# Kernel optimization log

Hardware: AMD Instinct MI355X
Metric: run time of the kernel (lower is better)

Reference implementation:

```python
import jax, jax.numpy as jnp
import numpy as np

B, S, D = 4, 2048, 1024
H = 16
HD = D // H  # 64


def setup_inputs() -> dict:
    key = jax.random.key(0)
    ks = jax.random.split(key, 5)
    std = 1.0 / np.sqrt(D)
    return {
        "x": jax.random.normal(ks[0], (B, S, D), dtype=jnp.float32),
        "Wq": jax.random.normal(ks[1], (D, D), dtype=jnp.float32) * std,
        "Wk": jax.random.normal(ks[2], (D, D), dtype=jnp.float32) * std,
        "Wv": jax.random.normal(ks[3], (D, D), dtype=jnp.float32) * std,
        "Wo": jax.random.normal(ks[4], (D, D), dtype=jnp.float32) * std,
        "bo": jnp.zeros((D,), dtype=jnp.float32),
    }


def reference(x, Wq, Wk, Wv, Wo, bo):
    b, n, d_in = x.shape
    q = (x @ Wq).reshape(b, n, H, HD).transpose(0, 2, 1, 3)  # [b,h,n,hd]
    k = (x @ Wk).reshape(b, n, H, HD).transpose(0, 2, 1, 3)
    v = (x @ Wv).reshape(b, n, H, HD).transpose(0, 2, 1, 3)
    scores = jnp.einsum("bhqd,bhkd->bhqk", q, k)  # full NxN, as in original
    causal = jnp.tril(jnp.ones((n, n), dtype=bool))  # True = keep
    scores = jnp.where(causal, scores, -jnp.inf)
    attn = jax.nn.softmax(scores / np.sqrt(HD), axis=-1)
    # dropout p=0.0 -> identity
    ctx = jnp.einsum("bhqk,bhkd->bqhd", attn, v).reshape(b, n, H * HD)
    return ctx @ Wo + bo
```

## Files before the change

### kernel.cpp

```cpp
#include <hip/hip_runtime.h>
#include <math.h>

#define BATCH 4
#define SLEN 2048
#define DMODEL 1024
#define NH 16
#define HD 64
#define MROWS (BATCH * SLEN)
#define QK_LD 2048

typedef __attribute__((ext_vector_type(8))) short short8;
typedef __attribute__((ext_vector_type(4))) float floatx4;

#define AS1 __attribute__((address_space(1)))
#define AS3 __attribute__((address_space(3)))

__device__ inline unsigned short f2bf(float f) {
    union { float f; unsigned u; } a; a.f = f;
    unsigned r = a.u + 0x7fff + ((a.u >> 16) & 1);
    return (unsigned short)(r >> 16);
}

__device__ inline unsigned pack_bf(float lo, float hi) {
    union { float f; unsigned u; } a, b; a.f = lo; b.f = hi;
    return __builtin_amdgcn_perm(b.u + 0x8000u, a.u + 0x8000u, 0x07060302u);
}
__device__ inline unsigned pack_tr(float lo, float hi) {
    union { float f; unsigned u; } a, b; a.f = lo; b.f = hi;
    return __builtin_amdgcn_perm(b.u, a.u, 0x07060302u);
}

__global__ __launch_bounds__(256) void cvt_all(
    const float* __restrict__ x,
    const float* __restrict__ Wq, const float* __restrict__ Wk,
    const float* __restrict__ Wv, const float* __restrict__ Wo,
    short* __restrict__ xb,
    short* __restrict__ WqkT, short* __restrict__ WvT, short* __restrict__ WoT)
{
    int bid = blockIdx.x;
    if (bid < 8192) {
        int i = (bid * 256 + threadIdx.x) * 4;
        float4 v = *(const float4*)(x + i);
        unsigned short t0 = f2bf(v.x), t1 = f2bf(v.y), t2 = f2bf(v.z), t3 = f2bf(v.w);
        uint2 o;
        o.x = (unsigned)t0 | ((unsigned)t1 << 16);
        o.y = (unsigned)t2 | ((unsigned)t3 << 16);
        *(uint2*)(xb + i) = o;
    } else {
        bid -= 8192;
        int z = bid >> 10;
        int inner = bid & 1023;
        int bxi = inner & 31, byi = inner >> 5;

        const float* W; short* Wt; float sc = 1.0f;
        if (z == 0)      { W = Wq; Wt = WqkT; sc = 0.18033688011112042f; }
        else if (z == 1) { W = Wk; Wt = WqkT + (size_t)DMODEL * DMODEL; }
        else if (z == 2) { W = Wv; Wt = WvT; }
        else             { W = Wo; Wt = WoT; }

        __shared__ float t[32][33];
        int bn = bxi * 32, bk = byi * 32;
        int tx = threadIdx.x & 31, r0 = (threadIdx.x >> 5) * 4;
        #pragma unroll
        for (int i = 0; i < 4; i++)
            t[r0 + i][tx] = W[(size_t)(bk + r0 + i) * DMODEL + bn + tx];
        __syncthreads();
        #pragma unroll
        for (int i = 0; i < 4; i++)
            Wt[(size_t)(bn + r0 + i) * DMODEL + bk + tx] = (short)f2bf(t[tx][r0 + i] * sc);
    }
}

#define TM 128
#define TN 128
#define TK 32

template <int OUT_BF16>
__device__ __forceinline__ void gemm_body(
    const short* __restrict__ A,
    const short* __restrict__ Bt,
    const float* __restrict__ bias,
    void* __restrict__ Cout, int N, int K, int m0, int n0)
{
    __shared__ short As[2][TM * TK];
    __shared__ short Bs[2][TN * TK];
    int tid = threadIdx.x;
    int l = tid & 63, w = tid >> 6;
    int wm = (w >> 1) * 64, wn = (w & 1) * 64;
    int lr = l & 15, lk = (l >> 4) * 8;

    const short* asrc[2];
    const short* bsrc[2];
    #pragma unroll
    for (int r = 0; r < 2; r++) {
        int c = r * 256 + tid;
        int mm = c >> 2, kk = (c & 3) * 8;
        asrc[r] = A  + (size_t)(m0 + mm) * K + kk;
        bsrc[r] = Bt + (size_t)(n0 + mm) * K + kk;
    }

    floatx4 acc[4][4] = {};

    #pragma unroll
    for (int r = 0; r < 2; r++) {
        int c = r * 256 + tid;
        __builtin_amdgcn_global_load_lds((const AS1 void*)asrc[r],
            (AS3 void*)(&As[0][0] + c * 8), 16, 0, 0);
        __builtin_amdgcn_global_load_lds((const AS1 void*)bsrc[r],
            (AS3 void*)(&Bs[0][0] + c * 8), 16, 0, 0);
        asrc[r] += TK; bsrc[r] += TK;
    }

    int nk = K / TK;
    for (int t = 0; t < nk; t++) {
        int cur = t & 1;
        if (t + 1 < nk) {
            #pragma unroll
            for (int r = 0; r < 2; r++) {
                int c = r * 256 + tid;
                __builtin_amdgcn_global_load_lds((const AS1 void*)asrc[r],
                    (AS3 void*)(&As[cur ^ 1][0] + c * 8), 16, 0, 0);
                __builtin_amdgcn_global_load_lds((const AS1 void*)bsrc[r],
                    (AS3 void*)(&Bs[cur ^ 1][0] + c * 8), 16, 0, 0);
                asrc[r] += TK; bsrc[r] += TK;
            }
            asm volatile("s_waitcnt vmcnt(4)" ::: "memory");
        } else {
            asm volatile("s_waitcnt vmcnt(0)" ::: "memory");
        }
        __builtin_amdgcn_s_barrier();
        __builtin_amdgcn_sched_barrier(0);

        short8 af[4], bg[4];
        #pragma unroll
        for (int i = 0; i < 4; i++) {
            af[i] = *(const short8*)(&As[cur][0] + (wm + i * 16 + lr) * TK + lk);
            bg[i] = *(const short8*)(&Bs[cur][0] + (wn + i * 16 + lr) * TK + lk);
        }
        #pragma unroll
        for (int mi = 0; mi < 4; mi++)
            #pragma unroll
            for (int ni = 0; ni < 4; ni++)
                acc[mi][ni] = __builtin_amdgcn_mfma_f32_16x16x32_bf16(
                    af[mi], bg[ni], acc[mi][ni], 0, 0, 0);

        __builtin_amdgcn_sched_barrier(0);
        __builtin_amdgcn_s_barrier();
    }

    int rbase = (l >> 4) * 4, cbase = l & 15;
    if (OUT_BF16) {
        short* C = (short*)Cout;
        #pragma unroll
        for (int mi = 0; mi < 4; mi++)
            #pragma unroll
            for (int r = 0; r < 4; r++) {
                int row = m0 + wm + mi * 16 + rbase + r;
                #pragma unroll
                for (int ni = 0; ni < 4; ni++) {
                    int col = n0 + wn + ni * 16 + cbase;
                    C[(size_t)row * N + col] = (short)f2bf(acc[mi][ni][r]);
                }
            }
    } else {
        float* C = (float*)Cout;
        #pragma unroll
        for (int mi = 0; mi < 4; mi++)
            #pragma unroll
            for (int r = 0; r < 4; r++) {
                int row = m0 + wm + mi * 16 + rbase + r;
                #pragma unroll
                for (int ni = 0; ni < 4; ni++) {
                    int col = n0 + wn + ni * 16 + cbase;
                    C[(size_t)row * N + col] = acc[mi][ni][r] + bias[col];
                }
            }
    }
}

template <int OUT_BF16>
__global__ __launch_bounds__(256) void mfma_gemm(
    const short* __restrict__ A, const short* __restrict__ Bt,
    const float* __restrict__ bias, void* __restrict__ Cout,
    int M, int N, int K)
{
    gemm_body<OUT_BF16>(A, Bt, bias, Cout, N, K, blockIdx.y * TM, blockIdx.x * TN);
}

__global__ __launch_bounds__(256) void qkv_gemm(
    const short* __restrict__ xb, const short* __restrict__ WqkT,
    const short* __restrict__ WvT, short* __restrict__ QKb,
    short* __restrict__ VtT)
{
    const short* A; const short* Bt; short* C; int N, m0, n0;
    int bid = blockIdx.x;
    if (bid < 1024) {
        A = xb; Bt = WqkT; C = QKb; N = 2048;
        m0 = (bid >> 4) * TM; n0 = (bid & 15) * TN;
    } else {
        int r = bid - 1024;
        A = WvT; Bt = xb; C = VtT; N = MROWS;
        m0 = (r >> 6) * TM; n0 = (r & 63) * TN;
    }
    gemm_body<1>(A, Bt, nullptr, C, N, DMODEL, m0, n0);
}

#define PSTR 72

__global__ __launch_bounds__(256, 4) void fa_mfma(
    const short* __restrict__ QK, const short* __restrict__ VtT,
    short* __restrict__ ctx)
{
    __shared__ __align__(16) short Ks[2][64][32];
    __shared__ __align__(16) short Vs[2][64][32];
    __shared__ __align__(16) short Ps[4][16][PSTR];

    int tid = threadIdx.x;
    int l = tid & 63, w = tid >> 6;
    int lr = l & 15, lg = l >> 4;
    int bh = blockIdx.x;
    int b = bh >> 4, h = bh & 15;
    int p = blockIdx.y;

    const short* Qbase = QK + (size_t)b * SLEN * QK_LD + h * HD;
    const short* Kbase = Qbase + 1024;
    const short* Vbase = VtT + (size_t)h * HD * MROWS + b * SLEN;

    int xoff = (lg ^ ((lr >> 1) & 3)) * 8;

    short8 ones;
    #pragma unroll
    for (int j = 0; j < 8; j++) ones[j] = (short)0x3F80;

    #pragma unroll 1
    for (int half = 0; half < 2; half++) {
        int qt = (half == 0) ? (31 - p) : p;
        int q0 = qt * 64;
        int qrow = q0 + w * 16 + lr;

        short8 qf[2];
        #pragma unroll
        for (int kk = 0; kk < 2; kk++)
            qf[kk] = *(const short8*)(Qbase + (size_t)qrow * QK_LD + kk * 32 + lg * 8);

        const short* ksrc[2];
        const short* vsrc[2];
        #pragma unroll
        for (int r2 = 0; r2 < 2; r2++) {
            int cc = r2 * 256 + tid;
            int kh = cc >> 8, rr = (cc >> 2) & 63;
            int q = (cc & 3) ^ ((rr >> 1) & 3);
            ksrc[r2] = Kbase + (size_t)rr * QK_LD + kh * 32 + q * 8;
            vsrc[r2] = Vbase + (size_t)rr * MROWS + kh * 32 + q * 8;
        }

        floatx4 O[4] = {};
        floatx4 accL = {};

        for (int kt = 0; kt <= qt; kt++) {
            int k0 = kt * 64;
            __syncthreads();
            #pragma unroll
            for (int r2 = 0; r2 < 2; r2++) {
                int cc = r2 * 256 + tid;
                __builtin_amdgcn_global_load_lds(
                    (const AS1 void*)ksrc[r2],
                    (AS3 void*)(&Ks[0][0][0] + cc * 8), 16, 0, 0);
                __builtin_amdgcn_global_load_lds(
                    (const AS1 void*)vsrc[r2],
                    (AS3 void*)(&Vs[0][0][0] + cc * 8), 16, 0, 0);
                ksrc[r2] += (size_t)64 * QK_LD;
                vsrc[r2] += 64;
            }
            __syncthreads();

            floatx4 s4[4] = {};
            #pragma unroll
            for (int kk = 0; kk < 2; kk++)
                #pragma unroll
                for (int t = 0; t < 4; t++) {
                    short8 kf = *(const short8*)(&Ks[kk][t * 16 + lr][xoff]);
                    s4[t] = __builtin_amdgcn_mfma_f32_16x16x32_bf16(kf, qf[kk], s4[t], 0, 0, 0);
                }

            if (kt == qt) {
                #pragma unroll
                for (int t = 0; t < 4; t++)
                    #pragma unroll
                    for (int r = 0; r < 4; r++)
                        if (k0 + t * 16 + lg * 4 + r > qrow) s4[t][r] = -INFINITY;
            }

            #pragma unroll
            for (int t = 0; t < 4; t++) {
                float p0 = __builtin_amdgcn_exp2f(s4[t][0]);
                float p1 = __builtin_amdgcn_exp2f(s4[t][1]);
                float p2 = __builtin_amdgcn_exp2f(s4[t][2]);
                float p3 = __builtin_amdgcn_exp2f(s4[t][3]);
                uint2 pk;
                pk.x = pack_tr(p0, p1);
                pk.y = pack_tr(p2, p3);
                *(uint2*)(&Ps[w][lr][t * 16 + lg * 4]) = pk;
            }

            #pragma unroll
            for (int kk = 0; kk < 2; kk++) {
                short8 pf = *(const short8*)(&Ps[w][lr][kk * 32 + lg * 8]);
                accL = __builtin_amdgcn_mfma_f32_16x16x32_bf16(ones, pf, accL, 0, 0, 0);
                #pragma unroll
                for (int dt = 0; dt < 4; dt++) {
                    short8 vf = *(const short8*)(&Vs[kk][dt * 16 + lr][xoff]);
                    O[dt] = __builtin_amdgcn_mfma_f32_16x16x32_bf16(vf, pf, O[dt], 0, 0, 0);
                }
            }
        }

        float linv = 1.f / accL[0];
        short* crow = ctx + ((size_t)b * SLEN + qrow) * DMODEL + h * HD;
        #pragma unroll
        for (int dt = 0; dt < 4; dt++) {
            uint2 pk;
            pk.x = pack_bf(O[dt][0] * linv, O[dt][1] * linv);
            pk.y = pack_bf(O[dt][2] * linv, O[dt][3] * linv);
            *(uint2*)(crow + dt * 16 + lg * 4) = pk;
        }
    }
}

extern "C" void kernel_launch(void* const* d_in, const int* in_sizes, int n_in,
                              void* d_out, int out_size, void* d_ws, size_t ws_size,
                              hipStream_t stream) {
    const float* x  = (const float*)d_in[0];
    const float* Wq = (const float*)d_in[1];
    const float* Wk = (const float*)d_in[2];
    const float* Wv = (const float*)d_in[3];
    const float* Wo = (const float*)d_in[4];
    const float* bo = (const float*)d_in[5];
    float* out = (float*)d_out;

    const size_t tsz = (size_t)MROWS * DMODEL;
    const size_t wsz = (size_t)DMODEL * DMODEL;

    short* xb    = (short*)d_ws;
    short* WqkT  = xb + tsz;
    short* WvT   = WqkT + 2 * wsz;
    short* WoT   = WvT + wsz;
    short* QKb   = WoT + wsz;
    short* VtT   = QKb + 2 * tsz;
    short* Cb    = VtT + tsz;

    cvt_all<<<12288, 256, 0, stream>>>(x, Wq, Wk, Wv, Wo, xb, WqkT, WvT, WoT);

    qkv_gemm<<<1536, 256, 0, stream>>>(xb, WqkT, WvT, QKb, VtT);

    fa_mfma<<<dim3(BATCH * NH, 16), 256, 0, stream>>>(QKb, VtT, Cb);

    mfma_gemm<0><<<dim3(DMODEL / TN, MROWS / TM), 256, 0, stream>>>(
        Cb, WoT, bo, out, MROWS, DMODEL, DMODEL);
}
```

Baseline: 243.1 us.

## Enlarge QKV GEMM tiles to 256x128 with 512-thread blocks

```diff
diff --git a/kernel.cpp b/kernel.cpp
--- a/kernel.cpp
+++ b/kernel.cpp
@@ -187,22 +187,106 @@
     gemm_body<OUT_BF16>(A, Bt, bias, Cout, N, K, blockIdx.y * TM, blockIdx.x * TN);
 }
 
-__global__ __launch_bounds__(256) void qkv_gemm(
+#define TM2 256
+#define TN2 128
+
+__global__ __launch_bounds__(512, 6) void qkv_gemm(
     const short* __restrict__ xb, const short* __restrict__ WqkT,
     const short* __restrict__ WvT, short* __restrict__ QKb,
     short* __restrict__ VtT)
 {
+    __shared__ short As[2][TM2 * TK];
+    __shared__ short Bs[2][TN2 * TK];
+
     const short* A; const short* Bt; short* C; int N, m0, n0;
     int bid = blockIdx.x;
-    if (bid < 1024) {
+    if (bid < 512) {
         A = xb; Bt = WqkT; C = QKb; N = 2048;
-        m0 = (bid >> 4) * TM; n0 = (bid & 15) * TN;
+        m0 = (bid >> 4) * TM2; n0 = (bid & 15) * TN2;
     } else {
-        int r = bid - 1024;
+        int r = bid - 512;
         A = WvT; Bt = xb; C = VtT; N = MROWS;
-        m0 = (r >> 6) * TM; n0 = (r & 63) * TN;
-    }
-    gemm_body<1>(A, Bt, nullptr, C, N, DMODEL, m0, n0);
+        m0 = (r >> 6) * TM2; n0 = (r & 63) * TN2;
+    }
+    const int K = DMODEL;
+
+    int tid = threadIdx.x;
+    int l = tid & 63, w = tid >> 6;
+    int wm = (w >> 1) * 64, wn = (w & 1) * 64;
+    int lr = l & 15, lk = (l >> 4) * 8;
+
+    const short* asrc[2];
+    const short* bsrc;
+    #pragma unroll
+    for (int r = 0; r < 2; r++) {
+        int c = r * 512 + tid;
+        asrc[r] = A + (size_t)(m0 + (c >> 2)) * K + (c & 3) * 8;
+    }
+    bsrc = Bt + (size_t)(n0 + (tid >> 2)) * K + (tid & 3) * 8;
+
+    floatx4 acc[4][4] = {};
+
+    #pragma unroll
+    for (int r = 0; r < 2; r++) {
+        int c = r * 512 + tid;
+        __builtin_amdgcn_global_load_lds((const AS1 void*)asrc[r],
+            (AS3 void*)(&As[0][0] + c * 8), 16, 0, 0);
+        asrc[r] += TK;
+    }
+    __builtin_amdgcn_global_load_lds((const AS1 void*)bsrc,
+        (AS3 void*)(&Bs[0][0] + tid * 8), 16, 0, 0);
+    bsrc += TK;
+
+    const int nk = K / TK;
+    for (int t = 0; t < nk; t++) {
+        int cur = t & 1;
+        if (t + 1 < nk) {
+            #pragma unroll
+            for (int r = 0; r < 2; r++) {
+                int c = r * 512 + tid;
+                __builtin_amdgcn_global_load_lds((const AS1 void*)asrc[r],
+                    (AS3 void*)(&As[cur ^ 1][0] + c * 8), 16, 0, 0);
+                asrc[r] += TK;
+            }
+            __builtin_amdgcn_global_load_lds((const AS1 void*)bsrc,
+                (AS3 void*)(&Bs[cur ^ 1][0] + tid * 8), 16, 0, 0);
+            bsrc += TK;
+            asm volatile("s_waitcnt vmcnt(3)" ::: "memory");
+        } else {
+            asm volatile("s_waitcnt vmcnt(0)" ::: "memory");
+        }
+        __builtin_amdgcn_s_barrier();
+        __builtin_amdgcn_sched_barrier(0);
+
+        short8 af[4], bg[4];
+        #pragma unroll
+        for (int i = 0; i < 4; i++) {
+            af[i] = *(const short8*)(&As[cur][0] + (wm + i * 16 + lr) * TK + lk);
+            bg[i] = *(const short8*)(&Bs[cur][0] + (wn + i * 16 + lr) * TK + lk);
+        }
+        #pragma unroll
+        for (int mi = 0; mi < 4; mi++)
+            #pragma unroll
+            for (int ni = 0; ni < 4; ni++)
+                acc[mi][ni] = __builtin_amdgcn_mfma_f32_16x16x32_bf16(
+                    af[mi], bg[ni], acc[mi][ni], 0, 0, 0);
+
+        __builtin_amdgcn_sched_barrier(0);
+        __builtin_amdgcn_s_barrier();
+    }
+
+    int rbase = (l >> 4) * 4, cbase = l & 15;
+    #pragma unroll
+    for (int mi = 0; mi < 4; mi++)
+        #pragma unroll
+        for (int r = 0; r < 4; r++) {
+            int row = m0 + wm + mi * 16 + rbase + r;
+            #pragma unroll
+            for (int ni = 0; ni < 4; ni++) {
+                int col = n0 + wn + ni * 16 + cbase;
+                C[(size_t)row * N + col] = (short)f2bf(acc[mi][ni][r]);
+            }
+        }
 }
 
 #define PSTR 72
@@ -351,7 +435,7 @@
 
     cvt_all<<<12288, 256, 0, stream>>>(x, Wq, Wk, Wv, Wo, xb, WqkT, WvT, WoT);
 
-    qkv_gemm<<<1536, 256, 0, stream>>>(xb, WqkT, WvT, QKb, VtT);
+    qkv_gemm<<<768, 512, 0, stream>>>(xb, WqkT, WvT, QKb, VtT);
 
     fa_mfma<<<dim3(BATCH * NH, 16), 256, 0, stream>>>(QKb, VtT, Cb);
 
```

Result: slower. 460.4 us (+89.3%).
